# Kernel tuning notes

Measured on AMD Instinct MI355X. Metric: run time of the kernel, lower is better.

The kernel has to match this reference:

```python
import jax, jax.numpy as jnp
import numpy as np

C = 256      # channels
G = 8        # groups
K = 9        # 3x3 sampling points (DCNv4 default kernel_size=3)
DWK = 3      # dw_kernel_size (wrapper passes kernel_size=3)
OFFSET_SCALE = 1.0
N, H, W = 8, 64, 64


def setup_inputs() -> dict:
    key = jax.random.key(0)
    ks = jax.random.split(key, 6)
    def init(k, shape, fan):
        return jax.random.normal(k, shape, jnp.float32) * (fan ** -0.5)
    return {
        "x": jax.random.normal(ks[0], (N, C, H, W), jnp.float32),
        "dw_w": init(ks[1], (C, 1, DWK, DWK), DWK * DWK),   # depthwise conv (OIHW, groups=C)
        "dw_b": jnp.zeros((C,), jnp.float32),
        "om_w": init(ks[2], (G * K * 3, C), C) * 0.01,       # offset/mask linear (small offsets)
        "om_b": jnp.zeros((G * K * 3,), jnp.float32),
        "vp_w": init(ks[3], (C, C), C),                      # value_proj
        "vp_b": jnp.zeros((C,), jnp.float32),
        "op_w": init(ks[4], (C, C), C),                      # output_proj (output_bias=False)
    }


def reference(x, dw_w, dw_b, om_w, om_b, vp_w, vp_b, op_w):
    n, c, h, w = x.shape
    cg = c // G
    L = h * w
    # b c h w -> b (h w) c
    xf = x.transpose(0, 2, 3, 1).reshape(n, L, c)
    value = (xf @ vp_w.T + vp_b).reshape(n, L, G, cg)
    # offset/mask branch: depthwise conv on raw input, then linear
    om_in = jax.lax.conv_general_dilated(
        x, dw_w, (1, 1), "SAME", feature_group_count=c,
        dimension_numbers=("NCHW", "OIHW", "NCHW")) + dw_b[None, :, None, None]
    om = om_in.transpose(0, 2, 3, 1).reshape(n, L, c) @ om_w.T + om_b  # (n, L, G*K*3)
    om = om.reshape(n, h, w, G, K * 3)
    off = om[..., : 2 * K].reshape(n, h, w, G, K, 2) * OFFSET_SCALE     # (dy, dx) per point
    mask = om[..., 2 * K:]                                              # (n,h,w,G,K) raw (DCNv4: no softmax)
    # base 3x3 dilation-1 grid centered at each pixel
    d = jnp.arange(-1, 2, dtype=jnp.float32)
    dy, dx = jnp.meshgrid(d, d, indexing="ij")
    base = jnp.stack([dy.ravel(), dx.ravel()], -1)  # (K, 2)
    py = (jnp.arange(h, dtype=jnp.float32).reshape(1, h, 1, 1, 1)
          + base[:, 0].reshape(1, 1, 1, 1, K) + off[..., 0])  # (n,h,w,G,K)
    px = (jnp.arange(w, dtype=jnp.float32).reshape(1, 1, w, 1, 1)
          + base[:, 1].reshape(1, 1, 1, 1, K) + off[..., 1])
    y0 = jnp.floor(py); x0 = jnp.floor(px)
    ty = py - y0; tx = px - x0
    y0i = y0.astype(jnp.int32); x0i = x0.astype(jnp.int32)

    def gather(yi, xi, wgt):
        valid = (yi >= 0) & (yi < h) & (xi >= 0) & (xi < w)
        idx = jnp.clip(yi, 0, h - 1) * w + jnp.clip(xi, 0, w - 1)       # (n,h,w,G,K)
        idx = idx.transpose(0, 1, 2, 4, 3).reshape(n, L * K, G)[..., None]
        g = jnp.take_along_axis(value, idx, axis=1)                     # (n, L*K, G, cg)
        g = g.reshape(n, h, w, K, G, cg).transpose(0, 1, 2, 4, 3, 5)    # (n,h,w,G,K,cg)
        return g * (wgt * valid)[..., None]

    sampled = (gather(y0i,     x0i,     (1 - ty) * (1 - tx))
             + gather(y0i,     x0i + 1, (1 - ty) * tx)
             + gather(y0i + 1, x0i,     ty * (1 - tx))
             + gather(y0i + 1, x0i + 1, ty * tx))
    out = jnp.einsum("nhwgk,nhwgkc->nhwgc", mask, sampled)  # mask-weighted aggregation
    out = out.reshape(n, L, c) @ op_w.T                      # output_proj (no bias)
    # b (h w) c -> b c h w
    return out.reshape(n, h, w, c).transpose(0, 3, 1, 2)
```

## Files before the change

kernel.cpp:

```cpp
#include <hip/hip_runtime.h>
#include <math.h>

#define N_  8
#define C_  256
#define G_  8
#define CG_ 32
#define K_  9
#define H_  64
#define W_  64
#define L_  (H_*W_)
#define OM_ 216
#define OMP_ 256

using frag_ab = __attribute__((ext_vector_type(8))) short;
using frag_cd = __attribute__((ext_vector_type(4))) float;

__device__ __forceinline__ unsigned short f2bf(float f) {
    unsigned int u = __float_as_uint(f);
    u += 0x7FFFu + ((u >> 16) & 1u);
    return (unsigned short)(u >> 16);
}
__device__ __forceinline__ float bflo(unsigned int u) { return __uint_as_float(u << 16); }
__device__ __forceinline__ float bfhi(unsigned int u) { return __uint_as_float(u & 0xFFFF0000u); }

__device__ __forceinline__ void gld16(const void* g, void* l) {
    __builtin_amdgcn_global_load_lds((const __attribute__((address_space(1))) void*)g,
                                     (__attribute__((address_space(3))) void*)l, 16, 0, 0);
}

__global__ __launch_bounds__(256) void prep_kernel(const float* __restrict__ x,
                                                   const float* __restrict__ w,
                                                   const float* __restrict__ b,
                                                   const float* __restrict__ vp_w,
                                                   const float* __restrict__ om_w,
                                                   const float* __restrict__ om_b,
                                                   const float* __restrict__ op_w,
                                                   unsigned short* __restrict__ xb,
                                                   unsigned short* __restrict__ omb,
                                                   unsigned short* __restrict__ vp_wb,
                                                   unsigned short* __restrict__ om_wb,
                                                   float* __restrict__ om_bp,
                                                   unsigned short* __restrict__ op_wb) {
    const int n = blockIdx.z, y = blockIdx.y, c0 = blockIdx.x * 32;
    const int tid = threadIdx.x;
    __shared__ float xs[3][32][66];
    __shared__ __align__(16) unsigned short os[2][64][40];
    if (tid < 192) {
        int r = tid / 64, c = (tid / 2) % 32, e = tid & 1;
        xs[r][c][e * 65] = 0.f;
    }
    const float* xbase = x + ((size_t)n * C_ + c0) * L_;
    for (int i = tid; i < 3 * 32 * 16; i += 256) {
        int r = i >> 9, rem = i & 511, c = rem >> 4, x4 = (rem & 15) * 4;
        int yy = y + r - 1;
        float4 v = make_float4(0.f, 0.f, 0.f, 0.f);
        if ((unsigned)yy < (unsigned)H_) v = *(const float4*)(xbase + (size_t)c * L_ + yy * W_ + x4);
        xs[r][c][1 + x4] = v.x; xs[r][c][2 + x4] = v.y;
        xs[r][c][3 + x4] = v.z; xs[r][c][4 + x4] = v.w;
    }
    __syncthreads();

    const int c = tid & 31, x0 = (tid >> 5) * 8;
    float wv[9];
#pragma unroll
    for (int i = 0; i < 9; i++) wv[i] = w[(c0 + c) * 9 + i];
    const float bias = b[c0 + c];
    float o[8];
#pragma unroll
    for (int j = 0; j < 8; j++) o[j] = bias;
#pragma unroll
    for (int r = 0; r < 3; r++) {
        float v[10];
#pragma unroll
        for (int d = 0; d < 10; d++) v[d] = xs[r][c][x0 + d];
#pragma unroll
        for (int j = 0; j < 8; j++)
            o[j] += wv[r * 3] * v[j] + wv[r * 3 + 1] * v[j + 1] + wv[r * 3 + 2] * v[j + 2];
    }
#pragma unroll
    for (int j = 0; j < 8; j++) {
        os[0][x0 + j][c] = f2bf(xs[1][c][1 + x0 + j]);
        os[1][x0 + j][c] = f2bf(o[j]);
    }
    __syncthreads();

    const int l = tid >> 2, c8 = (tid & 3) * 8;
    uint4 va = *(const uint4*)&os[0][l][c8];
    uint4 vc = *(const uint4*)&os[1][l][c8];
    size_t dst = ((size_t)n * L_ + y * W_ + l) * C_ + c0 + c8;
    *(uint4*)(xb + dst) = va;
    *(uint4*)(omb + dst) = vc;

    if (n == 0) {
        int idx = (blockIdx.x + 8 * blockIdx.y) * 256 + tid;
        if (idx < C_ * C_) {
            vp_wb[idx] = f2bf(vp_w[idx]);
            op_wb[idx] = f2bf(op_w[idx]);
            om_wb[idx] = (idx < OM_ * C_) ? f2bf(om_w[idx]) : (unsigned short)0;
        }
        if (idx < OMP_) om_bp[idx] = (idx < OM_) ? om_b[idx] : 0.f;
    }
}

__global__ __launch_bounds__(256) void gemm12_kernel(const unsigned short* __restrict__ xb,
                                                     const unsigned short* __restrict__ omb,
                                                     const unsigned short* __restrict__ vp_wb,
                                                     const unsigned short* __restrict__ om_wb,
                                                     const float* __restrict__ vp_b,
                                                     const float* __restrict__ om_bp,
                                                     unsigned short* __restrict__ valueb,
                                                     float* __restrict__ omf) {
    __shared__ unsigned short As[128 * 32];
    __shared__ unsigned short Bs[128 * 32];
    const int which = blockIdx.z;
    const unsigned short* A = which ? omb : xb;
    const unsigned short* B = which ? om_wb : vp_wb;
    const float* bias = which ? om_bp : vp_b;
    const int tid = threadIdx.x;
    const long i0 = (long)blockIdx.x * 128;
    const long j0 = (long)blockIdx.y * 128;
    const unsigned short* Ab = A + i0 * C_;
    const unsigned short* Bb = B + j0 * C_;
    const int wave = tid >> 6, lane = tid & 63;
    const int iw = (wave & 1) * 64, jw = (wave >> 1) * 64;
    const int lm = lane & 15, kq = lane >> 4;
    const int srow = tid >> 2, scol = (tid & 3) * 8;

    frag_cd acc[4][4];
#pragma unroll
    for (int a = 0; a < 4; a++)
#pragma unroll
        for (int c = 0; c < 4; c++) acc[a][c] = (frag_cd){0.f, 0.f, 0.f, 0.f};

    for (int k0 = 0; k0 < C_; k0 += 32) {
        const unsigned short* ga0 = Ab + (long)srow * C_ + k0 + scol;
        const unsigned short* gb0 = Bb + (long)srow * C_ + k0 + scol;
        gld16(ga0,            As + tid * 8);
        gld16(ga0 + 64 * C_,  As + 2048 + tid * 8);
        gld16(gb0,            Bs + tid * 8);
        gld16(gb0 + 64 * C_,  Bs + 2048 + tid * 8);
        __syncthreads();
        frag_ab af[4], bfr[4];
#pragma unroll
        for (int mi = 0; mi < 4; mi++)
            af[mi] = *(const frag_ab*)&As[(iw + mi * 16 + lm) * 32 + kq * 8];
#pragma unroll
        for (int ni = 0; ni < 4; ni++)
            bfr[ni] = *(const frag_ab*)&Bs[(jw + ni * 16 + lm) * 32 + kq * 8];
#pragma unroll
        for (int mi = 0; mi < 4; mi++)
#pragma unroll
            for (int ni = 0; ni < 4; ni++)
                acc[mi][ni] = __builtin_amdgcn_mfma_f32_16x16x32_bf16(af[mi], bfr[ni], acc[mi][ni], 0, 0, 0);
        __syncthreads();
    }

    float bv[4];
#pragma unroll
    for (int ni = 0; ni < 4; ni++)
        bv[ni] = bias[(int)(j0 + jw + ni * 16 + lm)];

    const long ibase = i0 + iw + kq * 4;
    const long jbase = j0 + jw + lm;
#pragma unroll
    for (int mi = 0; mi < 4; mi++) {
#pragma unroll
        for (int ni = 0; ni < 4; ni++) {
            long j = jbase + ni * 16;
#pragma unroll
            for (int r = 0; r < 4; r++) {
                long i = ibase + mi * 16 + r;
                float v = acc[mi][ni][r] + bv[ni];
                if (which)
                    omf[i * OMP_ + j] = v;
                else
                    valueb[i * C_ + j] = f2bf(v);
            }
        }
    }
}

__global__ __launch_bounds__(256, 3) void samplegemm_kernel(const unsigned short* __restrict__ value,
                                                            const float* __restrict__ om,
                                                            const unsigned short* __restrict__ opw,
                                                            float* __restrict__ out) {
    const int n = blockIdx.y, l0 = blockIdx.x * 64;
    const int tid = threadIdx.x;
    __shared__ __align__(16) unsigned short interm[64 * 256];
    __shared__ float4 wgt[64][9];
    __shared__ uint4  soff[64][9];

    const char* vbase = (const char*)(value + (size_t)n * L_ * C_);
    const int lp = tid >> 2;
    const int g = lp & 7;
    const int c8i = tid & 3;
    const int slot = tid & 31;
    const char* vb = vbase + (size_t)(g * CG_ + c8i * 8) * 2;

    for (int rep = 0; rep < 8; rep++) {
        __syncthreads();
        for (int it = tid; it < 576; it += 256) {
            int pl = it / 9, k = it - pl * 9;
            int p = rep * 8 + (pl >> 3), gg = pl & 7;
            int l = l0 + p, y = l >> 6, xp2 = l & 63;
            const float* so = om + ((size_t)n * L_ + l) * OMP_ + gg * 27;
            float offy = so[2 * k], offx = so[2 * k + 1], mk = so[18 + k];
            float py = (float)(y + k / 3 - 1) + offy;
            float px = (float)(xp2 + k % 3 - 1) + offx;
            float fy = floorf(py), fx = floorf(px);
            float ty = py - fy, tx = px - fx;
            int y0 = (int)fy, x0i = (int)fx;
            int y1 = y0 + 1, x1 = x0i + 1;
            float vy0 = ((unsigned)y0 < (unsigned)H_) ? 1.f : 0.f;
            float vy1 = ((unsigned)y1 < (unsigned)H_) ? 1.f : 0.f;
            float vx0 = ((unsigned)x0i < (unsigned)W_) ? 1.f : 0.f;
            float vx1 = ((unsigned)x1 < (unsigned)W_) ? 1.f : 0.f;
            int cy0 = min(max(y0, 0), H_ - 1), cy1 = min(max(y1, 0), H_ - 1);
            int cx0 = min(max(x0i, 0), W_ - 1), cx1 = min(max(x1, 0), W_ - 1);
            wgt[pl][k] = make_float4(mk * (1.f - ty) * (1.f - tx) * vy0 * vx0,
                                     mk * (1.f - ty) * tx         * vy0 * vx1,
                                     mk * ty         * (1.f - tx) * vy1 * vx0,
                                     mk * ty         * tx         * vy1 * vx1);
            soff[pl][k] = make_uint4((unsigned)((cy0 * W_ + cx0) << 9),
                                     (unsigned)((cy0 * W_ + cx1) << 9),
                                     (unsigned)((cy1 * W_ + cx0) << 9),
                                     (unsigned)((cy1 * W_ + cx1) << 9));
        }
        __syncthreads();
        const int p = rep * 8 + (lp >> 3);
        float acc[8] = {0.f, 0.f, 0.f, 0.f, 0.f, 0.f, 0.f, 0.f};
#pragma unroll
        for (int k = 0; k < K_; k++) {
            float4 wk = wgt[lp][k];
            uint4  ok = soff[lp][k];
            const uint4 v00 = *(const uint4*)(vb + ok.x);
            const uint4 v01 = *(const uint4*)(vb + ok.y);
            const uint4 v10 = *(const uint4*)(vb + ok.z);
            const uint4 v11 = *(const uint4*)(vb + ok.w);
#define ACC8(V, WW) { \
            acc[0] += WW * bflo(V.x); acc[1] += WW * bfhi(V.x); \
            acc[2] += WW * bflo(V.y); acc[3] += WW * bfhi(V.y); \
            acc[4] += WW * bflo(V.z); acc[5] += WW * bfhi(V.z); \
            acc[6] += WW * bflo(V.w); acc[7] += WW * bfhi(V.w); }
            ACC8(v00, wk.x) ACC8(v01, wk.y) ACC8(v10, wk.z) ACC8(v11, wk.w)
#undef ACC8
        }
        uint4 pk;
        unsigned short* ps = (unsigned short*)&pk;
#pragma unroll
        for (int i = 0; i < 8; i++) ps[i] = f2bf(acc[i]);
        int phys = slot ^ (p & 7);
        *(uint4*)&interm[p * 256 + phys * 8] = pk;
    }
    __syncthreads();

    const int wave = tid >> 6, lane = tid & 63;
    const int lm = lane & 15, kq = lane >> 4;
    const int q0w = wave * 64;
    frag_cd acc2[4][4];
#pragma unroll
    for (int a = 0; a < 4; a++)
#pragma unroll
        for (int c = 0; c < 4; c++) acc2[a][c] = (frag_cd){0.f, 0.f, 0.f, 0.f};

    for (int k0 = 0; k0 < C_; k0 += 32) {
        frag_ab af[4], bfr[4];
#pragma unroll
        for (int mi = 0; mi < 4; mi++)
            af[mi] = *(const frag_ab*)(opw + (size_t)(q0w + mi * 16 + lm) * C_ + k0 + kq * 8);
#pragma unroll
        for (int ni = 0; ni < 4; ni++) {
            int pxr = ni * 16 + lm;
            int phys = (k0 / 8 + kq) ^ (pxr & 7);
            bfr[ni] = *(const frag_ab*)&interm[pxr * 256 + phys * 8];
        }
#pragma unroll
        for (int mi = 0; mi < 4; mi++)
#pragma unroll
            for (int ni = 0; ni < 4; ni++)
                acc2[mi][ni] = __builtin_amdgcn_mfma_f32_16x16x32_bf16(af[mi], bfr[ni], acc2[mi][ni], 0, 0, 0);
    }

    float* ob = out + (size_t)n * C_ * L_ + l0;
#pragma unroll
    for (int mi = 0; mi < 4; mi++) {
#pragma unroll
        for (int ni = 0; ni < 4; ni++) {
            int pxr = ni * 16 + lm;
#pragma unroll
            for (int r = 0; r < 4; r++) {
                int q = q0w + mi * 16 + kq * 4 + r;
                ob[(size_t)q * L_ + pxr] = acc2[mi][ni][r];
            }
        }
    }
}

extern "C" void kernel_launch(void* const* d_in, const int* in_sizes, int n_in,
                              void* d_out, int out_size, void* d_ws, size_t ws_size,
                              hipStream_t stream) {
    const float* x    = (const float*)d_in[0];
    const float* dw_w = (const float*)d_in[1];
    const float* dw_b = (const float*)d_in[2];
    const float* om_w = (const float*)d_in[3];
    const float* om_b = (const float*)d_in[4];
    const float* vp_w = (const float*)d_in[5];
    const float* vp_b = (const float*)d_in[6];
    const float* op_w = (const float*)d_in[7];
    float* out = (float*)d_out;

    char* ws = (char*)d_ws;
    unsigned short* xb      = (unsigned short*)(ws);
    unsigned short* omb     = (unsigned short*)(ws + 16777216);
    unsigned short* valueb  = (unsigned short*)(ws + 33554432);
    float*          omf     = (float*)(ws + 50331648);
    unsigned short* vp_wb   = (unsigned short*)(ws + 83886080);
    unsigned short* om_wb   = (unsigned short*)(ws + 84017152);
    unsigned short* op_wb   = (unsigned short*)(ws + 84148224);
    float*          om_bp   = (float*)(ws + 84279296);

    prep_kernel<<<dim3(C_ / 32, H_, N_), 256, 0, stream>>>(
        x, dw_w, dw_b, vp_w, om_w, om_b, op_w,
        xb, omb, vp_wb, om_wb, om_bp, op_wb);
    gemm12_kernel<<<dim3(256, 2, 2), 256, 0, stream>>>(
        xb, omb, vp_wb, om_wb, vp_b, om_bp, valueb, omf);
    samplegemm_kernel<<<dim3(L_ / 64, N_), 256, 0, stream>>>(valueb, omf, op_wb, out);
}
```

Baseline: 170.9 us.

## Compute sampling weights per quad, prefetch offsets, halve pixel tile and reorder grid

The offset/mask output is now written with each group padded to 32 floats, so every quad of threads can load its own group's offsets with float2 reads. Each quad computes its own bilinear weights and indices into shared memory and prefetches the next rep's offsets. This removes the two block-wide barriers per rep and the cooperative division-heavy setup loop. The sampling+projection tile shrinks from 64 to 32 pixels, with launch bounds raised to 4 blocks per SM and the grid reordered so batch is the fast index. The trade-off is less reuse of op_w fragments per block, and the shared-memory hand-off now relies on ordering within a wave rather than an explicit barrier.

```diff
diff --git a/kernel.cpp b/kernel.cpp
--- a/kernel.cpp
+++ b/kernel.cpp
@@ -167,26 +167,29 @@
 #pragma unroll
         for (int ni = 0; ni < 4; ni++) {
             long j = jbase + ni * 16;
+            int jj = (int)j;
+            int gg = jj / 27, t = jj - gg * 27;
 #pragma unroll
             for (int r = 0; r < 4; r++) {
                 long i = ibase + mi * 16 + r;
                 float v = acc[mi][ni][r] + bv[ni];
-                if (which)
-                    omf[i * OMP_ + j] = v;
-                else
+                if (which) {
+                    if (jj < OM_) omf[i * OMP_ + gg * 32 + t] = v;
+                } else {
                     valueb[i * C_ + j] = f2bf(v);
+                }
             }
         }
     }
 }
 
-__global__ __launch_bounds__(256, 3) void samplegemm_kernel(const unsigned short* __restrict__ value,
+__global__ __launch_bounds__(256, 4) void samplegemm_kernel(const unsigned short* __restrict__ value,
                                                             const float* __restrict__ om,
                                                             const unsigned short* __restrict__ opw,
                                                             float* __restrict__ out) {
-    const int n = blockIdx.y, l0 = blockIdx.x * 64;
+    const int n = blockIdx.x, l0 = blockIdx.y * 32;
     const int tid = threadIdx.x;
-    __shared__ __align__(16) unsigned short interm[64 * 256];
+    __shared__ __align__(16) unsigned short interm[32 * 256];
     __shared__ float4 wgt[64][9];
     __shared__ uint4  soff[64][9];
 
@@ -197,37 +200,56 @@
     const int slot = tid & 31;
     const char* vb = vbase + (size_t)(g * CG_ + c8i * 8) * 2;
 
-    for (int rep = 0; rep < 8; rep++) {
-        __syncthreads();
-        for (int it = tid; it < 576; it += 256) {
-            int pl = it / 9, k = it - pl * 9;
-            int p = rep * 8 + (pl >> 3), gg = pl & 7;
-            int l = l0 + p, y = l >> 6, xp2 = l & 63;
-            const float* so = om + ((size_t)n * L_ + l) * OMP_ + gg * 27;
-            float offy = so[2 * k], offx = so[2 * k + 1], mk = so[18 + k];
-            float py = (float)(y + k / 3 - 1) + offy;
-            float px = (float)(xp2 + k % 3 - 1) + offx;
-            float fy = floorf(py), fx = floorf(px);
-            float ty = py - fy, tx = px - fx;
-            int y0 = (int)fy, x0i = (int)fx;
-            int y1 = y0 + 1, x1 = x0i + 1;
-            float vy0 = ((unsigned)y0 < (unsigned)H_) ? 1.f : 0.f;
-            float vy1 = ((unsigned)y1 < (unsigned)H_) ? 1.f : 0.f;
-            float vx0 = ((unsigned)x0i < (unsigned)W_) ? 1.f : 0.f;
-            float vx1 = ((unsigned)x1 < (unsigned)W_) ? 1.f : 0.f;
-            int cy0 = min(max(y0, 0), H_ - 1), cy1 = min(max(y1, 0), H_ - 1);
-            int cx0 = min(max(x0i, 0), W_ - 1), cx1 = min(max(x1, 0), W_ - 1);
-            wgt[pl][k] = make_float4(mk * (1.f - ty) * (1.f - tx) * vy0 * vx0,
-                                     mk * (1.f - ty) * tx         * vy0 * vx1,
-                                     mk * ty         * (1.f - tx) * vy1 * vx0,
-                                     mk * ty         * tx         * vy1 * vx1);
-            soff[pl][k] = make_uint4((unsigned)((cy0 * W_ + cx0) << 9),
-                                     (unsigned)((cy0 * W_ + cx1) << 9),
-                                     (unsigned)((cy1 * W_ + cx0) << 9),
-                                     (unsigned)((cy1 * W_ + cx1) << 9));
-        }
-        __syncthreads();
-        const int p = rep * 8 + (lp >> 3);
+    const int k0 = c8i * 3;
+    const int pin = lp >> 3;
+    const float* sob = om + ((size_t)n * L_ + l0 + pin) * OMP_ + g * 32;
+
+    float2 po01 = *(const float2*)(sob + 2 * k0);
+    float2 po23 = *(const float2*)(sob + 2 * k0 + 2);
+    float2 po45 = *(const float2*)(sob + 2 * k0 + 4);
+    float pmk0 = sob[18 + k0], pmk1 = sob[19 + k0], pmk2 = sob[20 + k0];
+
+    for (int rep = 0; rep < 4; rep++) {
+        const float oys[3] = {po01.x, po23.x, po45.x};
+        const float oxs[3] = {po01.y, po23.y, po45.y};
+        const float mks[3] = {pmk0, pmk1, pmk2};
+        if (rep < 3) {
+            const float* so = sob + (size_t)(rep + 1) * 8 * OMP_;
+            po01 = *(const float2*)(so + 2 * k0);
+            po23 = *(const float2*)(so + 2 * k0 + 2);
+            po45 = *(const float2*)(so + 2 * k0 + 4);
+            pmk0 = so[18 + k0]; pmk1 = so[19 + k0]; pmk2 = so[20 + k0];
+        }
+        const int p = rep * 8 + pin;
+        if (c8i < 3) {
+            const int l = l0 + p;
+            const int y = l >> 6, xp = l & 63;
+#pragma unroll
+            for (int j = 0; j < 3; j++) {
+                const int k = k0 + j;
+                float py = (float)(y + c8i - 1) + oys[j];
+                float px = (float)(xp + j - 1) + oxs[j];
+                float fy = floorf(py), fx = floorf(px);
+                float ty = py - fy, tx = px - fx;
+                int y0 = (int)fy, x0i = (int)fx;
+                int y1 = y0 + 1, x1 = x0i + 1;
+                float vy0 = ((unsigned)y0 < (unsigned)H_) ? 1.f : 0.f;
+                float vy1 = ((unsigned)y1 < (unsigned)H_) ? 1.f : 0.f;
+                float vx0 = ((unsigned)x0i < (unsigned)W_) ? 1.f : 0.f;
+                float vx1 = ((unsigned)x1 < (unsigned)W_) ? 1.f : 0.f;
+                int cy0 = min(max(y0, 0), H_ - 1), cy1 = min(max(y1, 0), H_ - 1);
+                int cx0 = min(max(x0i, 0), W_ - 1), cx1 = min(max(x1, 0), W_ - 1);
+                float mk = mks[j];
+                wgt[lp][k] = make_float4(mk * (1.f - ty) * (1.f - tx) * vy0 * vx0,
+                                         mk * (1.f - ty) * tx         * vy0 * vx1,
+                                         mk * ty         * (1.f - tx) * vy1 * vx0,
+                                         mk * ty         * tx         * vy1 * vx1);
+                soff[lp][k] = make_uint4((unsigned)((cy0 * W_ + cx0) << 9),
+                                         (unsigned)((cy0 * W_ + cx1) << 9),
+                                         (unsigned)((cy1 * W_ + cx0) << 9),
+                                         (unsigned)((cy1 * W_ + cx1) << 9));
+            }
+        }
         float acc[8] = {0.f, 0.f, 0.f, 0.f, 0.f, 0.f, 0.f, 0.f};
 #pragma unroll
         for (int k = 0; k < K_; k++) {
@@ -257,27 +279,27 @@
     const int wave = tid >> 6, lane = tid & 63;
     const int lm = lane & 15, kq = lane >> 4;
     const int q0w = wave * 64;
-    frag_cd acc2[4][4];
+    frag_cd acc2[4][2];
 #pragma unroll
     for (int a = 0; a < 4; a++)
 #pragma unroll
-        for (int c = 0; c < 4; c++) acc2[a][c] = (frag_cd){0.f, 0.f, 0.f, 0.f};
-
-    for (int k0 = 0; k0 < C_; k0 += 32) {
-        frag_ab af[4], bfr[4];
+        for (int c = 0; c < 2; c++) acc2[a][c] = (frag_cd){0.f, 0.f, 0.f, 0.f};
+
+    for (int kk = 0; kk < C_; kk += 32) {
+        frag_ab af[4], bfr[2];
 #pragma unroll
         for (int mi = 0; mi < 4; mi++)
-            af[mi] = *(const frag_ab*)(opw + (size_t)(q0w + mi * 16 + lm) * C_ + k0 + kq * 8);
-#pragma unroll
-        for (int ni = 0; ni < 4; ni++) {
+            af[mi] = *(const frag_ab*)(opw + (size_t)(q0w + mi * 16 + lm) * C_ + kk + kq * 8);
+#pragma unroll
+        for (int ni = 0; ni < 2; ni++) {
             int pxr = ni * 16 + lm;
-            int phys = (k0 / 8 + kq) ^ (pxr & 7);
+            int phys = (kk / 8 + kq) ^ (pxr & 7);
             bfr[ni] = *(const frag_ab*)&interm[pxr * 256 + phys * 8];
         }
 #pragma unroll
         for (int mi = 0; mi < 4; mi++)
 #pragma unroll
-            for (int ni = 0; ni < 4; ni++)
+            for (int ni = 0; ni < 2; ni++)
                 acc2[mi][ni] = __builtin_amdgcn_mfma_f32_16x16x32_bf16(af[mi], bfr[ni], acc2[mi][ni], 0, 0, 0);
     }
 
@@ -285,7 +307,7 @@
 #pragma unroll
     for (int mi = 0; mi < 4; mi++) {
 #pragma unroll
-        for (int ni = 0; ni < 4; ni++) {
+        for (int ni = 0; ni < 2; ni++) {
             int pxr = ni * 16 + lm;
 #pragma unroll
             for (int r = 0; r < 4; r++) {
@@ -324,5 +346,5 @@
         xb, omb, vp_wb, om_wb, om_bp, op_wb);
     gemm12_kernel<<<dim3(256, 2, 2), 256, 0, stream>>>(
         xb, omb, vp_wb, om_wb, vp_b, om_bp, valueb, omf);
-    samplegemm_kernel<<<dim3(L_ / 64, N_), 256, 0, stream>>>(valueb, omf, op_wb, out);
-}
+    samplegemm_kernel<<<dim3(N_, L_ / 32), 256, 0, stream>>>(valueb, omf, op_wb, out);
+}
```

After: 185.8 us. 8.7% more time.
